# Kernel tuning notes

Measured on AMD Instinct MI355X. Metric: run time of the kernel, lower is better.

## Reference

```python
import jax, jax.numpy as jnp
import numpy as np

B, S, N = 8, 2048, 1024

def setup_inputs() -> dict:
    key = jax.random.key(0)
    k1, k2, k3 = jax.random.split(key, 3)
    outer = jax.random.normal(k1, (B, S, N), dtype=jnp.float32)
    extended_attention_mask = jnp.zeros((B, 1, S), dtype=jnp.float32)
    # torch Linear init scale ~ 1/sqrt(n)
    sc = 1.0 / np.sqrt(N)
    Wk = jax.random.normal(k2, (N, N), dtype=jnp.float32) * sc
    bk = jnp.zeros((N,), dtype=jnp.float32)
    Wq = jax.random.normal(k3, (N, N), dtype=jnp.float32) * sc
    bq = jnp.zeros((N,), dtype=jnp.float32)
    return {"outer": outer, "extended_attention_mask": extended_attention_mask,
            "Wk": Wk, "bk": bk, "Wq": Wq, "bq": bq}

def reference(outer, extended_attention_mask, Wk, bk, Wq, bq):
    # k = sigmoid(outer @ Wk^T + bk), q = sigmoid(outer @ Wq^T + bq)
    k = jax.nn.sigmoid(jnp.einsum('bsn,mn->bsm', outer, Wk) + bk)  # [B,S,N]
    q = jax.nn.sigmoid(jnp.einsum('bsn,mn->bsm', outer, Wq) + bq)  # [B,S,N]
    # scores: q @ k^T + mask -> [B,S,S]
    s = jnp.einsum('bqn,bkn->bqk', q, k) + extended_attention_mask
    attn = jax.nn.softmax(s, axis=-1)
    out = jnp.einsum('bqk,bkn->bqn', attn, outer)  # [B,S,N]
    return out.sum(-1)  # [B,S]
```

## Files before the change

### kernel.cpp

```cpp
#include <hip/hip_runtime.h>
#include <hip/hip_bf16.h>

#define BB 8
#define SS 2048
#define NN 1024
#define MT (BB*SS)
#define NKC 16
#define NPC 32

typedef __attribute__((ext_vector_type(8))) short bf16x8;
typedef __attribute__((ext_vector_type(4))) float f32x4;
typedef unsigned short u16;
typedef unsigned int u32;

__device__ __forceinline__ u16 f2bf(float f) {
  u32 u = __float_as_uint(f);
  u += 0x7fff + ((u >> 16) & 1);
  return (u16)(u >> 16);
}
__device__ __forceinline__ float bf2f(u16 h) {
  return __uint_as_float(((u32)h) << 16);
}

typedef __attribute__((address_space(1))) void GV;
typedef __attribute__((address_space(3))) void LV;
__device__ __forceinline__ void cp16(const void* g, void* l) {
  __builtin_amdgcn_global_load_lds((GV*)g, (LV*)l, 16, 0, 0);
}

__global__ __launch_bounds__(256) void prep_x_kernel(const float* __restrict__ outer,
                                                     u16* __restrict__ Xb,
                                                     float* __restrict__ r) {
  int w = threadIdx.x >> 6, lane = threadIdx.x & 63;
  int row = blockIdx.x * 4 + w;
  const float4* src = (const float4*)(outer + (size_t)row * NN);
  ushort4* dst = (ushort4*)(Xb + (size_t)row * NN);
  float s = 0.f;
#pragma unroll
  for (int u = 0; u < 4; u++) {
    int idx = lane + u * 64;
    float4 v = src[idx];
    ushort4 o;
    o.x = f2bf(v.x); o.y = f2bf(v.y); o.z = f2bf(v.z); o.w = f2bf(v.w);
    dst[idx] = o;
    s += (v.x + v.y) + (v.z + v.w);
  }
#pragma unroll
  for (int off = 1; off < 64; off <<= 1) s += __shfl_xor(s, off);
  if (lane == 0) r[row] = s;
}

__global__ __launch_bounds__(256) void prep_w_kernel(const float* __restrict__ Wq,
                                                     const float* __restrict__ Wk,
                                                     const float* __restrict__ bq,
                                                     const float* __restrict__ bk,
                                                     u16* __restrict__ Wb,
                                                     float* __restrict__ bb) {
  int idx = blockIdx.x * 256 + threadIdx.x;
  int e = idx * 4;
  int rowm = e >> 10;
  int col = e & 1023;
  const float* srcp = (rowm < NN) ? (Wq + (size_t)rowm * NN + col)
                                  : (Wk + (size_t)(rowm - NN) * NN + col);
  float4 v = *(const float4*)srcp;
  ushort4 o; o.x = f2bf(v.x); o.y = f2bf(v.y); o.z = f2bf(v.z); o.w = f2bf(v.w);
  *(ushort4*)(Wb + (size_t)e) = o;
  if (idx < 2 * NN) bb[idx] = (idx < NN) ? bq[idx] : bk[idx - NN];
}

__global__ __launch_bounds__(256, 3) void gemm1_kernel(const u16* __restrict__ X,
                                                       const u16* __restrict__ W,
                                                       const float* __restrict__ bb,
                                                       u16* __restrict__ C) {
  __shared__ u16 lA[128 * 32];
  __shared__ u16 lB[128 * 32];
  int tn = blockIdx.x;
  int tm = blockIdx.y;
  int tid = threadIdx.x;
  int w = tid >> 6, lane = tid & 63;
  int wr = w >> 1, wc = w & 1;
  int srow = tid >> 2;
  int scol = (tid & 3) * 8;
  const u16* gA = X + (size_t)(tm * 128 + srow) * NN + scol;
  const u16* gB = W + (size_t)(tn * 128 + srow) * NN + scol;
  u16* dA = &lA[srow * 32 + scol];
  u16* dB = &lB[srow * 32 + scol];
  int quad = lane >> 4;
  const u16* pa0 = &lA[(wr * 64 + (lane & 15)) * 32 + quad * 8];
  const u16* pb0 = &lB[(wc * 64 + (lane & 15)) * 32 + quad * 8];
  f32x4 acc[4][4] = {};
  for (int kk = 0; kk < NN; kk += 32) {
    cp16(gA, dA);
    cp16(gA + 64 * NN, dA + 64 * 32);
    cp16(gB, dB);
    cp16(gB + 64 * NN, dB + 64 * 32);
    gA += 32; gB += 32;
    __syncthreads();
    bf16x8 af[4], bf[4];
#pragma unroll
    for (int i = 0; i < 4; i++) af[i] = *(const bf16x8*)(pa0 + i * 16 * 32);
#pragma unroll
    for (int j = 0; j < 4; j++) bf[j] = *(const bf16x8*)(pb0 + j * 16 * 32);
#pragma unroll
    for (int i = 0; i < 4; i++)
#pragma unroll
      for (int j = 0; j < 4; j++)
        acc[i][j] = __builtin_amdgcn_mfma_f32_16x16x32_bf16(af[i], bf[j], acc[i][j], 0, 0, 0);
    __syncthreads();
  }
  int quad4 = quad * 4;
  int colb = tn * 128 + wc * 64 + (lane & 15);
#pragma unroll
  for (int i = 0; i < 4; i++) {
#pragma unroll
    for (int j = 0; j < 4; j++) {
      int col = colb + j * 16;
      float bias = bb[col];
#pragma unroll
      for (int rg = 0; rg < 4; rg++) {
        int row = tm * 128 + wr * 64 + i * 16 + quad4 + rg;
        float v = acc[i][j][rg] + bias;
        float sg = 1.0f / (1.0f + __expf(-v));
        C[(size_t)row * 2048 + col] = f2bf(sg - 0.5f);
      }
    }
  }
}

__global__ __launch_bounds__(256) void kbias_kernel(const u16* __restrict__ C,
                                                    const float* __restrict__ mask,
                                                    float* __restrict__ kb) {
  int w = threadIdx.x >> 6, lane = threadIdx.x & 63;
  int row = blockIdx.x * 4 + w;
  const ushort4* src = (const ushort4*)(C + (size_t)row * 2048 + 1024);
  float s = 0.f;
#pragma unroll
  for (int u = 0; u < 4; u++) {
    ushort4 v = src[lane + u * 64];
    s += (bf2f(v.x) + bf2f(v.y)) + (bf2f(v.z) + bf2f(v.w));
  }
#pragma unroll
  for (int off = 1; off < 64; off <<= 1) s += __shfl_xor(s, off);
  if (lane == 0) kb[row] = 0.5f * s + mask[row];
}

__global__ __launch_bounds__(256, 3) void flash_kernel(const u16* __restrict__ C,
                                                       const float* __restrict__ kb,
                                                       const float* __restrict__ r,
                                                       float* __restrict__ pm,
                                                       float* __restrict__ pl,
                                                       float* __restrict__ pt) {
  __shared__ u16 lA[128 * 32];
  __shared__ u16 lB[128 * 32];
  int bid = blockIdx.x;
  int kc = bid & 15;
  int qt = (bid >> 4) & 15;
  int b  = bid >> 8;
  int tid = threadIdx.x;
  int w = tid >> 6, lane = tid & 63;
  int wr = w >> 1, wc = w & 1;
  int srow = tid >> 2;
  int scol = (tid & 3) * 8;
  int key0 = kc * 128;
  const u16* gA = C + (size_t)(b * SS + qt * 128 + srow) * 2048 + scol;
  const u16* gB = C + (size_t)(b * SS + key0 + srow) * 2048 + 1024 + scol;
  u16* dA = &lA[srow * 32 + scol];
  u16* dB = &lB[srow * 32 + scol];
  int quad = lane >> 4;
  const u16* pa0 = &lA[(wr * 64 + (lane & 15)) * 32 + quad * 8];
  const u16* pb0 = &lB[(wc * 64 + (lane & 15)) * 32 + quad * 8];

  f32x4 acc[4][4] = {};
  for (int kk = 0; kk < NN; kk += 32) {
    cp16(gA, dA);
    cp16(gA + 64 * 2048, dA + 64 * 32);
    cp16(gB, dB);
    cp16(gB + 64 * 2048, dB + 64 * 32);
    gA += 32; gB += 32;
    __syncthreads();
    bf16x8 af[4], bf[4];
#pragma unroll
    for (int i = 0; i < 4; i++) af[i] = *(const bf16x8*)(pa0 + i * 16 * 32);
#pragma unroll
    for (int j = 0; j < 4; j++) bf[j] = *(const bf16x8*)(pb0 + j * 16 * 32);
#pragma unroll
    for (int i = 0; i < 4; i++)
#pragma unroll
      for (int j = 0; j < 4; j++)
        acc[i][j] = __builtin_amdgcn_mfma_f32_16x16x32_bf16(af[i], bf[j], acc[i][j], 0, 0, 0);
    __syncthreads();
  }

  float kbv[4], rv[4];
  int colg = b * SS + key0 + wc * 64 + (lane & 15);
#pragma unroll
  for (int j = 0; j < 4; j++) { kbv[j] = kb[colg + j * 16]; rv[j] = r[colg + j * 16]; }
  int quad4 = quad * 4;
  int chunk = kc * 2 + wc;
#pragma unroll
  for (int i = 0; i < 4; i++) {
#pragma unroll
    for (int rg = 0; rg < 4; rg++) {
      float lg[4];
      float tmax = -1e30f;
#pragma unroll
      for (int j = 0; j < 4; j++) { lg[j] = acc[i][j][rg] + kbv[j]; tmax = fmaxf(tmax, lg[j]); }
#pragma unroll
      for (int off = 1; off < 16; off <<= 1) tmax = fmaxf(tmax, __shfl_xor(tmax, off));
      float rs = 0.f, rt = 0.f;
#pragma unroll
      for (int j = 0; j < 4; j++) {
        float p = __expf(lg[j] - tmax);
        rs += p; rt += p * rv[j];
      }
#pragma unroll
      for (int off = 1; off < 16; off <<= 1) { rs += __shfl_xor(rs, off); rt += __shfl_xor(rt, off); }
      if ((lane & 15) == 0) {
        int grow = b * SS + qt * 128 + wr * 64 + i * 16 + quad4 + rg;
        pm[grow * NPC + chunk] = tmax;
        pl[grow * NPC + chunk] = rs;
        pt[grow * NPC + chunk] = rt;
      }
    }
  }
}

__global__ __launch_bounds__(256) void fixup_kernel(const float* __restrict__ pm,
                                                    const float* __restrict__ pl,
                                                    const float* __restrict__ pt,
                                                    float* __restrict__ out) {
  int row = blockIdx.x * 256 + threadIdx.x;
  float Mx = -1e30f;
#pragma unroll
  for (int c = 0; c < NPC; c++) Mx = fmaxf(Mx, pm[row * NPC + c]);
  float L = 0.f, T = 0.f;
#pragma unroll
  for (int c = 0; c < NPC; c++) {
    float a = __expf(pm[row * NPC + c] - Mx);
    L += pl[row * NPC + c] * a;
    T += pt[row * NPC + c] * a;
  }
  out[row] = T / L;
}

extern "C" void kernel_launch(void* const* d_in, const int* in_sizes, int n_in,
                              void* d_out, int out_size, void* d_ws, size_t ws_size,
                              hipStream_t stream) {
  const float* outer = (const float*)d_in[0];
  const float* mask  = (const float*)d_in[1];
  const float* Wk    = (const float*)d_in[2];
  const float* bk    = (const float*)d_in[3];
  const float* Wq    = (const float*)d_in[4];
  const float* bq    = (const float*)d_in[5];
  float* out = (float*)d_out;

  char* ws = (char*)d_ws;
  size_t off = 0;
  auto alloc = [&](size_t bytes) -> void* {
    void* p = ws + off;
    off = (off + bytes + 255) & ~(size_t)255;
    return p;
  };
  u16* Xb  = (u16*)alloc((size_t)MT * NN * 2);
  u16* Wb  = (u16*)alloc((size_t)2048 * NN * 2);
  u16* Cq  = (u16*)alloc((size_t)MT * 2048 * 2);
  float* bb = (float*)alloc(2048 * 4);
  float* rr = (float*)alloc((size_t)MT * 4);
  float* kb = (float*)alloc((size_t)MT * 4);
  float* pm = (float*)alloc((size_t)MT * NPC * 4);
  float* pl = (float*)alloc((size_t)MT * NPC * 4);
  float* pt = (float*)alloc((size_t)MT * NPC * 4);

  prep_x_kernel<<<dim3(MT / 4), dim3(256), 0, stream>>>(outer, Xb, rr);
  prep_w_kernel<<<dim3(2048), dim3(256), 0, stream>>>(Wq, Wk, bq, bk, Wb, bb);
  gemm1_kernel<<<dim3(16, 128), dim3(256), 0, stream>>>(Xb, Wb, bb, Cq);
  kbias_kernel<<<dim3(MT / 4), dim3(256), 0, stream>>>(Cq, mask, kb);
  flash_kernel<<<dim3(8 * 16 * NKC), dim3(256), 0, stream>>>(Cq, kb, rr, pm, pl, pt);
  fixup_kernel<<<dim3(MT / 256), dim3(256), 0, stream>>>(pm, pl, pt, out);
}
```

Before: 307.5 us.

## Fuse key-bias row sums into GEMM epilogue, widen K step, remap block order

```diff
diff --git a/kernel.cpp b/kernel.cpp
--- a/kernel.cpp
+++ b/kernel.cpp
@@ -29,8 +29,10 @@
 }
 
 __global__ __launch_bounds__(256) void prep_x_kernel(const float* __restrict__ outer,
+                                                     const float* __restrict__ mask,
                                                      u16* __restrict__ Xb,
-                                                     float* __restrict__ r) {
+                                                     float* __restrict__ r,
+                                                     float* __restrict__ kb) {
   int w = threadIdx.x >> 6, lane = threadIdx.x & 63;
   int row = blockIdx.x * 4 + w;
   const float4* src = (const float4*)(outer + (size_t)row * NN);
@@ -47,7 +49,7 @@
   }
 #pragma unroll
   for (int off = 1; off < 64; off <<= 1) s += __shfl_xor(s, off);
-  if (lane == 0) r[row] = s;
+  if (lane == 0) { r[row] = s; kb[row] = mask[row]; }
 }
 
 __global__ __launch_bounds__(256) void prep_w_kernel(const float* __restrict__ Wq,
@@ -71,11 +73,13 @@
 __global__ __launch_bounds__(256, 3) void gemm1_kernel(const u16* __restrict__ X,
                                                        const u16* __restrict__ W,
                                                        const float* __restrict__ bb,
-                                                       u16* __restrict__ C) {
-  __shared__ u16 lA[128 * 32];
-  __shared__ u16 lB[128 * 32];
-  int tn = blockIdx.x;
-  int tm = blockIdx.y;
+                                                       u16* __restrict__ C,
+                                                       float* __restrict__ kb) {
+  __shared__ u16 lA[2][128 * 32];
+  __shared__ u16 lB[2][128 * 32];
+  int bid = blockIdx.x;
+  int tn = ((bid & 7) << 1) | ((bid >> 3) & 1);
+  int tm = bid >> 4;
   int tid = threadIdx.x;
   int w = tid >> 6, lane = tid & 63;
   int wr = w >> 1, wc = w & 1;
@@ -83,35 +87,55 @@
   int scol = (tid & 3) * 8;
   const u16* gA = X + (size_t)(tm * 128 + srow) * NN + scol;
   const u16* gB = W + (size_t)(tn * 128 + srow) * NN + scol;
-  u16* dA = &lA[srow * 32 + scol];
-  u16* dB = &lB[srow * 32 + scol];
+  u16* dA0 = &lA[0][srow * 32 + scol];
+  u16* dA1 = &lA[1][srow * 32 + scol];
+  u16* dB0 = &lB[0][srow * 32 + scol];
+  u16* dB1 = &lB[1][srow * 32 + scol];
   int quad = lane >> 4;
-  const u16* pa0 = &lA[(wr * 64 + (lane & 15)) * 32 + quad * 8];
-  const u16* pb0 = &lB[(wc * 64 + (lane & 15)) * 32 + quad * 8];
+  const u16* pa0 = &lA[0][(wr * 64 + (lane & 15)) * 32 + quad * 8];
+  const u16* pb0 = &lB[0][(wc * 64 + (lane & 15)) * 32 + quad * 8];
+  const u16* pa1 = pa0 + 128 * 32;
+  const u16* pb1 = pb0 + 128 * 32;
   f32x4 acc[4][4] = {};
-  for (int kk = 0; kk < NN; kk += 32) {
-    cp16(gA, dA);
-    cp16(gA + 64 * NN, dA + 64 * 32);
-    cp16(gB, dB);
-    cp16(gB + 64 * NN, dB + 64 * 32);
-    gA += 32; gB += 32;
+  for (int kk = 0; kk < NN; kk += 64) {
+    cp16(gA, dA0);           cp16(gA + 64 * NN, dA0 + 64 * 32);
+    cp16(gB, dB0);           cp16(gB + 64 * NN, dB0 + 64 * 32);
+    cp16(gA + 32, dA1);      cp16(gA + 32 + 64 * NN, dA1 + 64 * 32);
+    cp16(gB + 32, dB1);      cp16(gB + 32 + 64 * NN, dB1 + 64 * 32);
+    gA += 64; gB += 64;
     __syncthreads();
-    bf16x8 af[4], bf[4];
-#pragma unroll
-    for (int i = 0; i < 4; i++) af[i] = *(const bf16x8*)(pa0 + i * 16 * 32);
-#pragma unroll
-    for (int j = 0; j < 4; j++) bf[j] = *(const bf16x8*)(pb0 + j * 16 * 32);
-#pragma unroll
-    for (int i = 0; i < 4; i++)
-#pragma unroll
-      for (int j = 0; j < 4; j++)
-        acc[i][j] = __builtin_amdgcn_mfma_f32_16x16x32_bf16(af[i], bf[j], acc[i][j], 0, 0, 0);
+    {
+      bf16x8 af[4], bf[4];
+#pragma unroll
+      for (int i = 0; i < 4; i++) af[i] = *(const bf16x8*)(pa0 + i * 16 * 32);
+#pragma unroll
+      for (int j = 0; j < 4; j++) bf[j] = *(const bf16x8*)(pb0 + j * 16 * 32);
+#pragma unroll
+      for (int i = 0; i < 4; i++)
+#pragma unroll
+        for (int j = 0; j < 4; j++)
+          acc[i][j] = __builtin_amdgcn_mfma_f32_16x16x32_bf16(af[i], bf[j], acc[i][j], 0, 0, 0);
+    }
+    {
+      bf16x8 af[4], bf[4];
+#pragma unroll
+      for (int i = 0; i < 4; i++) af[i] = *(const bf16x8*)(pa1 + i * 16 * 32);
+#pragma unroll
+      for (int j = 0; j < 4; j++) bf[j] = *(const bf16x8*)(pb1 + j * 16 * 32);
+#pragma unroll
+      for (int i = 0; i < 4; i++)
+#pragma unroll
+        for (int j = 0; j < 4; j++)
+          acc[i][j] = __builtin_amdgcn_mfma_f32_16x16x32_bf16(af[i], bf[j], acc[i][j], 0, 0, 0);
+    }
     __syncthreads();
   }
   int quad4 = quad * 4;
   int colb = tn * 128 + wc * 64 + (lane & 15);
+  bool khalf = (tn >= 8);
 #pragma unroll
   for (int i = 0; i < 4; i++) {
+    float rsum[4] = {0.f, 0.f, 0.f, 0.f};
 #pragma unroll
     for (int j = 0; j < 4; j++) {
       int col = colb + j * 16;
@@ -121,27 +145,24 @@
         int row = tm * 128 + wr * 64 + i * 16 + quad4 + rg;
         float v = acc[i][j][rg] + bias;
         float sg = 1.0f / (1.0f + __expf(-v));
-        C[(size_t)row * 2048 + col] = f2bf(sg - 0.5f);
+        u16 h = f2bf(sg - 0.5f);
+        C[(size_t)row * 2048 + col] = h;
+        rsum[rg] += bf2f(h);
       }
     }
-  }
-}
-
-__global__ __launch_bounds__(256) void kbias_kernel(const u16* __restrict__ C,
-                                                    const float* __restrict__ mask,
-                                                    float* __restrict__ kb) {
-  int w = threadIdx.x >> 6, lane = threadIdx.x & 63;
-  int row = blockIdx.x * 4 + w;
-  const ushort4* src = (const ushort4*)(C + (size_t)row * 2048 + 1024);
-  float s = 0.f;
-#pragma unroll
-  for (int u = 0; u < 4; u++) {
-    ushort4 v = src[lane + u * 64];
-    s += (bf2f(v.x) + bf2f(v.y)) + (bf2f(v.z) + bf2f(v.w));
-  }
-#pragma unroll
-  for (int off = 1; off < 64; off <<= 1) s += __shfl_xor(s, off);
-  if (lane == 0) kb[row] = 0.5f * s + mask[row];
+    if (khalf) {
+#pragma unroll
+      for (int rg = 0; rg < 4; rg++) {
+        float s = rsum[rg];
+#pragma unroll
+        for (int off = 1; off < 16; off <<= 1) s += __shfl_xor(s, off);
+        if ((lane & 15) == 0) {
+          int row = tm * 128 + wr * 64 + i * 16 + quad4 + rg;
+          atomicAdd(&kb[row], 0.5f * s);
+        }
+      }
+    }
+  }
 }
 
 __global__ __launch_bounds__(256, 3) void flash_kernel(const u16* __restrict__ C,
@@ -150,12 +171,12 @@
                                                        float* __restrict__ pm,
                                                        float* __restrict__ pl,
                                                        float* __restrict__ pt) {
-  __shared__ u16 lA[128 * 32];
-  __shared__ u16 lB[128 * 32];
+  __shared__ u16 lA[2][128 * 32];
+  __shared__ u16 lB[2][128 * 32];
   int bid = blockIdx.x;
-  int kc = bid & 15;
-  int qt = (bid >> 4) & 15;
-  int b  = bid >> 8;
+  int b  = bid & 7;
+  int kc = (bid >> 3) & 15;
+  int qt = bid >> 7;
   int tid = threadIdx.x;
   int w = tid >> 6, lane = tid & 63;
   int wr = w >> 1, wc = w & 1;
@@ -164,30 +185,48 @@
   int key0 = kc * 128;
   const u16* gA = C + (size_t)(b * SS + qt * 128 + srow) * 2048 + scol;
   const u16* gB = C + (size_t)(b * SS + key0 + srow) * 2048 + 1024 + scol;
-  u16* dA = &lA[srow * 32 + scol];
-  u16* dB = &lB[srow * 32 + scol];
+  u16* dA0 = &lA[0][srow * 32 + scol];
+  u16* dA1 = &lA[1][srow * 32 + scol];
+  u16* dB0 = &lB[0][srow * 32 + scol];
+  u16* dB1 = &lB[1][srow * 32 + scol];
   int quad = lane >> 4;
-  const u16* pa0 = &lA[(wr * 64 + (lane & 15)) * 32 + quad * 8];
-  const u16* pb0 = &lB[(wc * 64 + (lane & 15)) * 32 + quad * 8];
+  const u16* pa0 = &lA[0][(wr * 64 + (lane & 15)) * 32 + quad * 8];
+  const u16* pb0 = &lB[0][(wc * 64 + (lane & 15)) * 32 + quad * 8];
+  const u16* pa1 = pa0 + 128 * 32;
+  const u16* pb1 = pb0 + 128 * 32;
 
   f32x4 acc[4][4] = {};
-  for (int kk = 0; kk < NN; kk += 32) {
-    cp16(gA, dA);
-    cp16(gA + 64 * 2048, dA + 64 * 32);
-    cp16(gB, dB);
-    cp16(gB + 64 * 2048, dB + 64 * 32);
-    gA += 32; gB += 32;
+  for (int kk = 0; kk < NN; kk += 64) {
+    cp16(gA, dA0);           cp16(gA + 64 * 2048, dA0 + 64 * 32);
+    cp16(gB, dB0);           cp16(gB + 64 * 2048, dB0 + 64 * 32);
+    cp16(gA + 32, dA1);      cp16(gA + 32 + 64 * 2048, dA1 + 64 * 32);
+    cp16(gB + 32, dB1);      cp16(gB + 32 + 64 * 2048, dB1 + 64 * 32);
+    gA += 64; gB += 64;
     __syncthreads();
-    bf16x8 af[4], bf[4];
-#pragma unroll
-    for (int i = 0; i < 4; i++) af[i] = *(const bf16x8*)(pa0 + i * 16 * 32);
-#pragma unroll
-    for (int j = 0; j < 4; j++) bf[j] = *(const bf16x8*)(pb0 + j * 16 * 32);
-#pragma unroll
-    for (int i = 0; i < 4; i++)
-#pragma unroll
-      for (int j = 0; j < 4; j++)
-        acc[i][j] = __builtin_amdgcn_mfma_f32_16x16x32_bf16(af[i], bf[j], acc[i][j], 0, 0, 0);
+    {
+      bf16x8 af[4], bf[4];
+#pragma unroll
+      for (int i = 0; i < 4; i++) af[i] = *(const bf16x8*)(pa0 + i * 16 * 32);
+#pragma unroll
+      for (int j = 0; j < 4; j++) bf[j] = *(const bf16x8*)(pb0 + j * 16 * 32);
+#pragma unroll
+      for (int i = 0; i < 4; i++)
+#pragma unroll
+        for (int j = 0; j < 4; j++)
+          acc[i][j] = __builtin_amdgcn_mfma_f32_16x16x32_bf16(af[i], bf[j], acc[i][j], 0, 0, 0);
+    }
+    {
+      bf16x8 af[4], bf[4];
+#pragma unroll
+      for (int i = 0; i < 4; i++) af[i] = *(const bf16x8*)(pa1 + i * 16 * 32);
+#pragma unroll
+      for (int j = 0; j < 4; j++) bf[j] = *(const bf16x8*)(pb1 + j * 16 * 32);
+#pragma unroll
+      for (int i = 0; i < 4; i++)
+#pragma unroll
+        for (int j = 0; j < 4; j++)
+          acc[i][j] = __builtin_amdgcn_mfma_f32_16x16x32_bf16(af[i], bf[j], acc[i][j], 0, 0, 0);
+    }
     __syncthreads();
   }
 
@@ -271,10 +310,9 @@
   float* pl = (float*)alloc((size_t)MT * NPC * 4);
   float* pt = (float*)alloc((size_t)MT * NPC * 4);
 
-  prep_x_kernel<<<dim3(MT / 4), dim3(256), 0, stream>>>(outer, Xb, rr);
+  prep_x_kernel<<<dim3(MT / 4), dim3(256), 0, stream>>>(outer, mask, Xb, rr, kb);
   prep_w_kernel<<<dim3(2048), dim3(256), 0, stream>>>(Wq, Wk, bq, bk, Wb, bb);
-  gemm1_kernel<<<dim3(16, 128), dim3(256), 0, stream>>>(Xb, Wb, bb, Cq);
-  kbias_kernel<<<dim3(MT / 4), dim3(256), 0, stream>>>(Cq, mask, kb);
-  flash_kernel<<<dim3(8 * 16 * NKC), dim3(256), 0, stream>>>(Cq, kb, rr, pm, pl, pt);
+  gemm1_kernel<<<dim3(2048), dim3(256), 0, stream>>>(Xb, Wb, bb, Cq, kb);
+  flash_kernel<<<dim3(2048), dim3(256), 0, stream>>>(Cq, kb, rr, pm, pl, pt);
   fixup_kernel<<<dim3(MT / 256), dim3(256), 0, stream>>>(pm, pl, pt, out);
 }
```

Measured after the change: 293.6 us. 4.5% less time.

## Fuse key-bias reduction into GEMM epilogue, swizzle LDS, remap block order

Applied to the files above, without the earlier changes.

```diff
diff --git a/kernel.cpp b/kernel.cpp
--- a/kernel.cpp
+++ b/kernel.cpp
@@ -5,7 +5,6 @@
 #define SS 2048
 #define NN 1024
 #define MT (BB*SS)
-#define NKC 16
 #define NPC 32
 
 typedef __attribute__((ext_vector_type(8))) short bf16x8;
@@ -29,8 +28,10 @@
 }
 
 __global__ __launch_bounds__(256) void prep_x_kernel(const float* __restrict__ outer,
+                                                     const float* __restrict__ mask,
                                                      u16* __restrict__ Xb,
-                                                     float* __restrict__ r) {
+                                                     float* __restrict__ r,
+                                                     float* __restrict__ kb) {
   int w = threadIdx.x >> 6, lane = threadIdx.x & 63;
   int row = blockIdx.x * 4 + w;
   const float4* src = (const float4*)(outer + (size_t)row * NN);
@@ -47,7 +48,7 @@
   }
 #pragma unroll
   for (int off = 1; off < 64; off <<= 1) s += __shfl_xor(s, off);
-  if (lane == 0) r[row] = s;
+  if (lane == 0) { r[row] = s; kb[row] = mask[row]; }
 }
 
 __global__ __launch_bounds__(256) void prep_w_kernel(const float* __restrict__ Wq,
@@ -71,23 +72,27 @@
 __global__ __launch_bounds__(256, 3) void gemm1_kernel(const u16* __restrict__ X,
                                                        const u16* __restrict__ W,
                                                        const float* __restrict__ bb,
-                                                       u16* __restrict__ C) {
+                                                       u16* __restrict__ C,
+                                                       float* __restrict__ kb) {
   __shared__ u16 lA[128 * 32];
   __shared__ u16 lB[128 * 32];
-  int tn = blockIdx.x;
-  int tm = blockIdx.y;
+  int bid = blockIdx.x;
+  int tn = ((bid & 7) << 1) | ((bid >> 3) & 1);
+  int tm = bid >> 4;
   int tid = threadIdx.x;
   int w = tid >> 6, lane = tid & 63;
   int wr = w >> 1, wc = w & 1;
   int srow = tid >> 2;
-  int scol = (tid & 3) * 8;
-  const u16* gA = X + (size_t)(tm * 128 + srow) * NN + scol;
-  const u16* gB = W + (size_t)(tn * 128 + srow) * NN + scol;
-  u16* dA = &lA[srow * 32 + scol];
-  u16* dB = &lB[srow * 32 + scol];
+  int gchunk = (tid & 3) ^ ((tid >> 3) & 3);
+  const u16* gA = X + (size_t)(tm * 128 + srow) * NN + gchunk * 8;
+  const u16* gB = W + (size_t)(tn * 128 + srow) * NN + gchunk * 8;
+  u16* dA = &lA[srow * 32 + (tid & 3) * 8];
+  u16* dB = &lB[srow * 32 + (tid & 3) * 8];
   int quad = lane >> 4;
-  const u16* pa0 = &lA[(wr * 64 + (lane & 15)) * 32 + quad * 8];
-  const u16* pb0 = &lB[(wc * 64 + (lane & 15)) * 32 + quad * 8];
+  int rl = lane & 15;
+  int sw = quad ^ ((rl >> 1) & 3);
+  const u16* pa0 = &lA[(wr * 64 + rl) * 32 + sw * 8];
+  const u16* pb0 = &lB[(wc * 64 + rl) * 32 + sw * 8];
   f32x4 acc[4][4] = {};
   for (int kk = 0; kk < NN; kk += 32) {
     cp16(gA, dA);
@@ -109,9 +114,11 @@
     __syncthreads();
   }
   int quad4 = quad * 4;
-  int colb = tn * 128 + wc * 64 + (lane & 15);
+  int colb = tn * 128 + wc * 64 + rl;
+  bool khalf = (tn >= 8);
 #pragma unroll
   for (int i = 0; i < 4; i++) {
+    float rsum[4] = {0.f, 0.f, 0.f, 0.f};
 #pragma unroll
     for (int j = 0; j < 4; j++) {
       int col = colb + j * 16;
@@ -121,27 +128,24 @@
         int row = tm * 128 + wr * 64 + i * 16 + quad4 + rg;
         float v = acc[i][j][rg] + bias;
         float sg = 1.0f / (1.0f + __expf(-v));
-        C[(size_t)row * 2048 + col] = f2bf(sg - 0.5f);
+        u16 h = f2bf(sg - 0.5f);
+        C[(size_t)row * 2048 + col] = h;
+        rsum[rg] += bf2f(h);
       }
     }
-  }
-}
-
-__global__ __launch_bounds__(256) void kbias_kernel(const u16* __restrict__ C,
-                                                    const float* __restrict__ mask,
-                                                    float* __restrict__ kb) {
-  int w = threadIdx.x >> 6, lane = threadIdx.x & 63;
-  int row = blockIdx.x * 4 + w;
-  const ushort4* src = (const ushort4*)(C + (size_t)row * 2048 + 1024);
-  float s = 0.f;
-#pragma unroll
-  for (int u = 0; u < 4; u++) {
-    ushort4 v = src[lane + u * 64];
-    s += (bf2f(v.x) + bf2f(v.y)) + (bf2f(v.z) + bf2f(v.w));
-  }
-#pragma unroll
-  for (int off = 1; off < 64; off <<= 1) s += __shfl_xor(s, off);
-  if (lane == 0) kb[row] = 0.5f * s + mask[row];
+    if (khalf) {
+#pragma unroll
+      for (int rg = 0; rg < 4; rg++) {
+        float s = rsum[rg];
+#pragma unroll
+        for (int off = 1; off < 16; off <<= 1) s += __shfl_xor(s, off);
+        if (rl == 0) {
+          int row = tm * 128 + wr * 64 + i * 16 + quad4 + rg;
+          atomicAdd(&kb[row], 0.5f * s);
+        }
+      }
+    }
+  }
 }
 
 __global__ __launch_bounds__(256, 3) void flash_kernel(const u16* __restrict__ C,
@@ -153,22 +157,24 @@
   __shared__ u16 lA[128 * 32];
   __shared__ u16 lB[128 * 32];
   int bid = blockIdx.x;
-  int kc = bid & 15;
-  int qt = (bid >> 4) & 15;
-  int b  = bid >> 8;
+  int b  = bid & 7;
+  int kc = (bid >> 3) & 15;
+  int qt = bid >> 7;
   int tid = threadIdx.x;
   int w = tid >> 6, lane = tid & 63;
   int wr = w >> 1, wc = w & 1;
   int srow = tid >> 2;
-  int scol = (tid & 3) * 8;
+  int gchunk = (tid & 3) ^ ((tid >> 3) & 3);
   int key0 = kc * 128;
-  const u16* gA = C + (size_t)(b * SS + qt * 128 + srow) * 2048 + scol;
-  const u16* gB = C + (size_t)(b * SS + key0 + srow) * 2048 + 1024 + scol;
-  u16* dA = &lA[srow * 32 + scol];
-  u16* dB = &lB[srow * 32 + scol];
+  const u16* gA = C + (size_t)(b * SS + qt * 128 + srow) * 2048 + gchunk * 8;
+  const u16* gB = C + (size_t)(b * SS + key0 + srow) * 2048 + 1024 + gchunk * 8;
+  u16* dA = &lA[srow * 32 + (tid & 3) * 8];
+  u16* dB = &lB[srow * 32 + (tid & 3) * 8];
   int quad = lane >> 4;
-  const u16* pa0 = &lA[(wr * 64 + (lane & 15)) * 32 + quad * 8];
-  const u16* pb0 = &lB[(wc * 64 + (lane & 15)) * 32 + quad * 8];
+  int rl = lane & 15;
+  int sw = quad ^ ((rl >> 1) & 3);
+  const u16* pa0 = &lA[(wr * 64 + rl) * 32 + sw * 8];
+  const u16* pb0 = &lB[(wc * 64 + rl) * 32 + sw * 8];
 
   f32x4 acc[4][4] = {};
   for (int kk = 0; kk < NN; kk += 32) {
@@ -192,7 +198,7 @@
   }
 
   float kbv[4], rv[4];
-  int colg = b * SS + key0 + wc * 64 + (lane & 15);
+  int colg = b * SS + key0 + wc * 64 + rl;
 #pragma unroll
   for (int j = 0; j < 4; j++) { kbv[j] = kb[colg + j * 16]; rv[j] = r[colg + j * 16]; }
   int quad4 = quad * 4;
@@ -215,7 +221,7 @@
       }
 #pragma unroll
       for (int off = 1; off < 16; off <<= 1) { rs += __shfl_xor(rs, off); rt += __shfl_xor(rt, off); }
-      if ((lane & 15) == 0) {
+      if (rl == 0) {
         int grow = b * SS + qt * 128 + wr * 64 + i * 16 + quad4 + rg;
         pm[grow * NPC + chunk] = tmax;
         pl[grow * NPC + chunk] = rs;
@@ -271,10 +277,9 @@
   float* pl = (float*)alloc((size_t)MT * NPC * 4);
   float* pt = (float*)alloc((size_t)MT * NPC * 4);
 
-  prep_x_kernel<<<dim3(MT / 4), dim3(256), 0, stream>>>(outer, Xb, rr);
+  prep_x_kernel<<<dim3(MT / 4), dim3(256), 0, stream>>>(outer, mask, Xb, rr, kb);
   prep_w_kernel<<<dim3(2048), dim3(256), 0, stream>>>(Wq, Wk, bq, bk, Wb, bb);
-  gemm1_kernel<<<dim3(16, 128), dim3(256), 0, stream>>>(Xb, Wb, bb, Cq);
-  kbias_kernel<<<dim3(MT / 4), dim3(256), 0, stream>>>(Cq, mask, kb);
-  flash_kernel<<<dim3(8 * 16 * NKC), dim3(256), 0, stream>>>(Cq, kb, rr, pm, pl, pt);
+  gemm1_kernel<<<dim3(2048), dim3(256), 0, stream>>>(Xb, Wb, bb, Cq, kb);
+  flash_kernel<<<dim3(2048), dim3(256), 0, stream>>>(Cq, kb, rr, pm, pl, pt);
   fixup_kernel<<<dim3(MT / 256), dim3(256), 0, stream>>>(pm, pl, pt, out);
 }
```

New measurement: 302.5 us. Within noise of the previous version (-1.6%).
